# Performance work log

Hardware: AMD Instinct MI355X
Metric: run time of the kernel (lower is better)

Reference implementation:

```python
import jax, jax.numpy as jnp
import numpy as np

D_IN = 1024
D_OUT = 1024
NUM_HEADS = 16
HEAD_DIM = D_OUT // NUM_HEADS


def setup_inputs() -> dict:
    key = jax.random.key(0)
    k_x, k_qkv, k_pw, k_pb = jax.random.split(key, 4)
    x = jax.random.normal(k_x, (2, 2048, D_IN), dtype=jnp.float32)
    # torch nn.Linear(d_in, 3*d_out, bias=False): weight [3*d_out, d_in]
    w_qkv = jax.random.normal(k_qkv, (3 * D_OUT, D_IN), dtype=jnp.float32) * (1.0 / np.sqrt(D_IN))
    # proj: nn.Linear(d_out, d_out) with bias
    w_proj = jax.random.normal(k_pw, (D_OUT, D_OUT), dtype=jnp.float32) * (1.0 / np.sqrt(D_OUT))
    b_proj = jax.random.normal(k_pb, (D_OUT,), dtype=jnp.float32) * 0.01
    return {"x": x, "w_qkv": w_qkv, "w_proj": w_proj, "b_proj": b_proj}


def reference(x, w_qkv, w_proj, b_proj):
    B, S, _ = x.shape
    # fused QKV projection: [B,S,3*D_OUT]
    qkv = jnp.einsum('bsd,ed->bse', x, w_qkv)
    qkv = qkv.reshape(B, S, 3, NUM_HEADS, HEAD_DIM)
    q, k, v = jnp.moveaxis(qkv, 2, 0)  # each [B,S,H,Dh]
    scale = 1.0 / jnp.sqrt(jnp.asarray(HEAD_DIM, dtype=x.dtype))
    # scores [B,H,S,S]
    scores = jnp.einsum('bqhd,bkhd->bhqk', q, k) * scale
    causal = jnp.tril(jnp.ones((S, S), dtype=bool))
    scores = jnp.where(causal, scores, jnp.asarray(-jnp.inf, dtype=scores.dtype))
    attn = jax.nn.softmax(scores, axis=-1)
    ctx = jnp.einsum('bhqk,bkhd->bqhd', attn, v)  # [B,S,H,Dh]
    ctx = ctx.reshape(B, S, D_OUT)
    return jnp.einsum('bsd,ed->bse', ctx, w_proj) + b_proj
```

## Files before the change

kernel.cpp:

```cpp
#include <hip/hip_runtime.h>
#include <hip/hip_bf16.h>
#include <cstdint>

#define B_SZ   2
#define S_LEN  2048
#define NH     16
#define NT     32
#define LDA    72

using f32x4 = __attribute__((ext_vector_type(4))) float;
typedef __bf16 bf16x8 __attribute__((ext_vector_type(8)));
typedef __bf16 bf16x4 __attribute__((ext_vector_type(4)));

__device__ inline float bf2f(unsigned short u) {
    union { unsigned int i; float f; } v; v.i = ((unsigned int)u) << 16; return v.f;
}
__device__ inline unsigned short f2bf(float f) {
    union { float f; unsigned int i; } v; v.f = f;
    unsigned int r = v.i + 0x7fff + ((v.i >> 16) & 1);
    return (unsigned short)(r >> 16);
}
__device__ inline f32x4 mfma16(bf16x8 a, bf16x8 b, f32x4 c) {
    return __builtin_amdgcn_mfma_f32_16x16x32_bf16(a, b, c, 0, 0, 0);
}
__device__ inline void stC(float* C, size_t idx, float v)  { C[idx] = v; }
__device__ inline void stC(__bf16* C, size_t idx, float v) { ((unsigned short*)C)[idx] = f2bf(v); }

__global__ __launch_bounds__(256) void f2b2_kernel(
    const float* __restrict__ a, int na4, __bf16* __restrict__ outa,
    const float* __restrict__ b, int nb4, __bf16* __restrict__ outb)
{
    int i = blockIdx.x * blockDim.x + threadIdx.x;
    const float* src; __bf16* dst; int idx;
    if (i < na4)           { src = a; dst = outa; idx = i; }
    else if (i < na4 + nb4){ src = b; dst = outb; idx = i - na4; }
    else return;
    float4 v = ((const float4*)src)[idx];
    ushort4 o;
    o.x = f2bf(v.x); o.y = f2bf(v.y); o.z = f2bf(v.z); o.w = f2bf(v.w);
    ((ushort4*)dst)[idx] = o;
}

__global__ __launch_bounds__(256) void f2b_kernel(
    const float* __restrict__ in, __bf16* __restrict__ out, int n4)
{
    int i = blockIdx.x * blockDim.x + threadIdx.x;
    if (i < n4) {
        float4 v = ((const float4*)in)[i];
        ushort4 o;
        o.x = f2bf(v.x); o.y = f2bf(v.y); o.z = f2bf(v.z); o.w = f2bf(v.w);
        ((ushort4*)out)[i] = o;
    }
}

template <typename TO, int HAS_BIAS>
__global__ __launch_bounds__(256) void gemm128(
    const __bf16* __restrict__ A, const __bf16* __restrict__ W,
    const float* __restrict__ bias, TO* __restrict__ C,
    int M, int N, int K)
{
    __shared__ __bf16 Alds[2][128 * 32];
    __shared__ __bf16 Blds[2][128 * 32];
    const int tid  = threadIdx.x, lane = tid & 63, w = tid >> 6;
    const int c16  = lane & 15, quad = lane >> 4;
    const int mBase = blockIdx.y * 128, nBase = blockIdx.x * 128;
    const int moff = (w & 1) * 64, noff = (w >> 1) * 64;

    f32x4 acc[4][4];
#pragma unroll
    for (int i = 0; i < 4; ++i)
#pragma unroll
        for (int j = 0; j < 4; ++j) acc[i][j] = (f32x4){0.f, 0.f, 0.f, 0.f};

    auto stage = [&](int buf, int k0) {
#pragma unroll
        for (int p = 0; p < 2; ++p) {
            const int linear = p * 256 + tid;
            const int row = linear >> 2;
            const int seg = (linear & 3) ^ (row & 3);
            const int lbase = (p * 256 + w * 64) * 8;
            const __bf16* ga = A + (size_t)(mBase + row) * K + k0 + seg * 8;
            const __bf16* gb = W + (size_t)(nBase + row) * K + k0 + seg * 8;
            __builtin_amdgcn_global_load_lds(
                (const __attribute__((address_space(1))) void*)ga,
                (__attribute__((address_space(3))) void*)(&Alds[buf][lbase]), 16, 0, 0);
            __builtin_amdgcn_global_load_lds(
                (const __attribute__((address_space(1))) void*)gb,
                (__attribute__((address_space(3))) void*)(&Blds[buf][lbase]), 16, 0, 0);
        }
    };

    stage(0, 0);
    int cur = 0;
    for (int k0 = 0; k0 < K; k0 += 32) {
        __syncthreads();
        if (k0 + 32 < K) stage(cur ^ 1, k0 + 32);

        bf16x8 af[4], bw[4];
#pragma unroll
        for (int i = 0; i < 4; ++i) {
            const int rowA = moff + i * 16 + c16;
            af[i] = *(const bf16x8*)&Alds[cur][rowA * 32 + ((quad ^ (rowA & 3)) << 3)];
            const int rowB = noff + i * 16 + c16;
            bw[i] = *(const bf16x8*)&Blds[cur][rowB * 32 + ((quad ^ (rowB & 3)) << 3)];
        }
#pragma unroll
        for (int i = 0; i < 4; ++i)
#pragma unroll
            for (int j = 0; j < 4; ++j)
                acc[i][j] = mfma16(af[i], bw[j], acc[i][j]);
        cur ^= 1;
    }

#pragma unroll
    for (int j = 0; j < 4; ++j) {
        const int col = nBase + noff + j * 16 + c16;
        const float bv = HAS_BIAS ? bias[col] : 0.f;
#pragma unroll
        for (int i = 0; i < 4; ++i)
#pragma unroll
            for (int r = 0; r < 4; ++r) {
                const int row = mBase + moff + i * 16 + quad * 4 + r;
                stC(C, (size_t)row * N + col, acc[i][j][r] + bv);
            }
    }
}

template <typename TO, int HAS_BIAS>
__global__ __launch_bounds__(256) void gemm64(
    const __bf16* __restrict__ A, const __bf16* __restrict__ W,
    const float* __restrict__ bias, TO* __restrict__ C,
    int M, int N, int K)
{
    __shared__ __bf16 Alds[2][64 * 32];
    __shared__ __bf16 Blds[2][128 * 32];
    const int tid  = threadIdx.x, lane = tid & 63, w = tid >> 6;
    const int c16  = lane & 15, quad = lane >> 4;
    const int mBase = blockIdx.y * 64, nBase = blockIdx.x * 128;
    const int moff = (w & 1) * 32, noff = (w >> 1) * 64;

    f32x4 acc[2][4];
#pragma unroll
    for (int i = 0; i < 2; ++i)
#pragma unroll
        for (int j = 0; j < 4; ++j) acc[i][j] = (f32x4){0.f, 0.f, 0.f, 0.f};

    auto stage = [&](int buf, int k0) {
        {
            const int row = tid >> 2;
            const int seg = (tid & 3) ^ (row & 3);
            const int lbase = (w * 64) * 8;
            const __bf16* ga = A + (size_t)(mBase + row) * K + k0 + seg * 8;
            __builtin_amdgcn_global_load_lds(
                (const __attribute__((address_space(1))) void*)ga,
                (__attribute__((address_space(3))) void*)(&Alds[buf][lbase]), 16, 0, 0);
        }
#pragma unroll
        for (int p = 0; p < 2; ++p) {
            const int linear = p * 256 + tid;
            const int row = linear >> 2;
            const int seg = (linear & 3) ^ (row & 3);
            const int lbase = (p * 256 + w * 64) * 8;
            const __bf16* gb = W + (size_t)(nBase + row) * K + k0 + seg * 8;
            __builtin_amdgcn_global_load_lds(
                (const __attribute__((address_space(1))) void*)gb,
                (__attribute__((address_space(3))) void*)(&Blds[buf][lbase]), 16, 0, 0);
        }
    };

    stage(0, 0);
    int cur = 0;
    for (int k0 = 0; k0 < K; k0 += 32) {
        __syncthreads();
        if (k0 + 32 < K) stage(cur ^ 1, k0 + 32);

        bf16x8 af[2], bw[4];
#pragma unroll
        for (int i = 0; i < 2; ++i) {
            const int rowA = moff + i * 16 + c16;
            af[i] = *(const bf16x8*)&Alds[cur][rowA * 32 + ((quad ^ (rowA & 3)) << 3)];
        }
#pragma unroll
        for (int j = 0; j < 4; ++j) {
            const int rowB = noff + j * 16 + c16;
            bw[j] = *(const bf16x8*)&Blds[cur][rowB * 32 + ((quad ^ (rowB & 3)) << 3)];
        }
#pragma unroll
        for (int i = 0; i < 2; ++i)
#pragma unroll
            for (int j = 0; j < 4; ++j)
                acc[i][j] = mfma16(af[i], bw[j], acc[i][j]);
        cur ^= 1;
    }

#pragma unroll
    for (int j = 0; j < 4; ++j) {
        const int col = nBase + noff + j * 16 + c16;
        const float bv = HAS_BIAS ? bias[col] : 0.f;
#pragma unroll
        for (int i = 0; i < 2; ++i)
#pragma unroll
            for (int r = 0; r < 4; ++r) {
                const int row = mBase + moff + i * 16 + quad * 4 + r;
                stC(C, (size_t)row * N + col, acc[i][j][r] + bv);
            }
    }
}

__global__ __launch_bounds__(256) void attn(
    const __bf16* __restrict__ qkv, __bf16* __restrict__ ctx,
    float* __restrict__ opart, float* __restrict__ lpart)
{
    __shared__ __bf16 Qs[64 * LDA];
    __shared__ __bf16 Ks[64 * LDA];
    __shared__ __bf16 Vs[64 * LDA];
    __shared__ __bf16 Ps[64 * LDA];

    const int tid  = threadIdx.x;
    const int lane = tid & 63;
    const int w    = tid >> 6;
    const int c16  = lane & 15;
    const int quad = lane >> 4;
    const int bh = blockIdx.x, b = bh >> 4, h = bh & 15;
    const int y  = blockIdx.y;

    int qt, c0, c1, seg;
    bool split;
    if (y < 16)      { qt = 16 + y; const int half = (qt + 2) >> 1; c0 = 0;    c1 = half;   split = true;  seg = 0; }
    else if (y < 32) { qt = y;      const int half = (qt + 2) >> 1; c0 = half; c1 = qt + 1; split = true;  seg = 1; }
    else             { qt = 47 - y; c0 = 0; c1 = qt + 1; split = false; seg = 0; }
    const int qBase = qt * 64;
    const int segIdx = split ? ((bh * 16 + (qt - 16)) * 2 + seg) : 0;

    const float QS = 0.125f * 1.4426950408889634f;

    const int krow0 = tid >> 3;
    const int kd0   = (tid & 7) * 8;
    const int c16t = tid & 15;
    const int jh   = (tid >> 4) & 1;
    const int dblk = tid >> 5;

    const size_t rowB = (size_t)b * S_LEN;
    const __bf16* kp0 = qkv + (rowB + c0 * 64 + krow0) * 3072 + 1024 + h * 64 + kd0;
    const __bf16* kp1 = kp0 + (size_t)32 * 3072;
    const __bf16* vp0 = qkv + (rowB + c0 * 64 + 2 * jh * 16 + c16t) * 3072 + 2048 + h * 64 + dblk * 8;
    const __bf16* vp1 = vp0 + (size_t)16 * 3072;

    uint4 kr0 = *(const uint4*)kp0;
    uint4 kr1 = *(const uint4*)kp1;
    uint4 vr0 = *(const uint4*)vp0;
    uint4 vr1 = *(const uint4*)vp1;

#pragma unroll
    for (int p = 0; p < 2; ++p) {
        const int linear = p * 256 + tid;
        const int row = linear >> 3;
        const int d0 = (linear & 7) * 8;
        const __bf16* g = qkv + (rowB + qBase + row) * 3072 + h * 64 + d0;
        uint4 raw = *(const uint4*)g;
        const unsigned short* u = (const unsigned short*)&raw;
        unsigned short tmp[8];
#pragma unroll
        for (int jj = 0; jj < 8; ++jj) tmp[jj] = f2bf(bf2f(u[jj]) * QS);
        *(uint4*)&Qs[row * LDA + d0] = *(const uint4*)tmp;
    }
    __syncthreads();

    const bf16x8 aq0 = *(const bf16x8*)&Qs[(w * 16 + c16) * LDA + quad * 8];
    const bf16x8 aq1 = *(const bf16x8*)&Qs[(w * 16 + c16) * LDA + 32 + quad * 8];

    float l_r[4] = {0.f, 0.f, 0.f, 0.f};
    f32x4 acc_o[4];
#pragma unroll
    for (int j = 0; j < 4; ++j) acc_o[j] = (f32x4){0.f, 0.f, 0.f, 0.f};

    for (int cc = c0; cc < c1; ++cc) {
        *(uint4*)&Ks[krow0 * LDA + kd0]        = kr0;
        *(uint4*)&Ks[(krow0 + 32) * LDA + kd0] = kr1;
        {
            const unsigned short* e1 = (const unsigned short*)&vr0;
            const unsigned short* e2 = (const unsigned short*)&vr1;
#pragma unroll
            for (int d = 0; d < 8; ++d) {
                const unsigned pack = (unsigned)e1[d] | ((unsigned)e2[d] << 16);
                *(unsigned*)&Vs[(dblk * 8 + d) * LDA + c16t * 4 + 2 * jh] = pack;
            }
        }
        __syncthreads();

        if (cc + 1 < c1) {
            kp0 += (size_t)64 * 3072; kp1 += (size_t)64 * 3072;
            vp0 += (size_t)64 * 3072; vp1 += (size_t)64 * 3072;
            kr0 = *(const uint4*)kp0;
            kr1 = *(const uint4*)kp1;
            vr0 = *(const uint4*)vp0;
            vr1 = *(const uint4*)vp1;
        }

        f32x4 sc[4];
#pragma unroll
        for (int j = 0; j < 4; ++j) sc[j] = (f32x4){0.f, 0.f, 0.f, 0.f};
#pragma unroll
        for (int j = 0; j < 4; ++j) {
            bf16x8 bk0 = *(const bf16x8*)&Ks[(j * 16 + c16) * LDA + quad * 8];
            bf16x8 bk1 = *(const bf16x8*)&Ks[(j * 16 + c16) * LDA + 32 + quad * 8];
            sc[j] = mfma16(aq0, bk0, sc[j]);
            sc[j] = mfma16(aq1, bk1, sc[j]);
        }

        if (cc == qt) {
#pragma unroll
            for (int j = 0; j < 4; ++j) {
                const int key = cc * 64 + j * 16 + c16;
#pragma unroll
                for (int r = 0; r < 4; ++r) {
                    const int q = qBase + w * 16 + quad * 4 + r;
                    if (key > q) sc[j][r] = -1e30f;
                }
            }
        }

        float p_[4][4];
#pragma unroll
        for (int j = 0; j < 4; ++j)
#pragma unroll
            for (int r = 0; r < 4; ++r)
                p_[j][r] = exp2f(sc[j][r]);
#pragma unroll
        for (int r = 0; r < 4; ++r)
            l_r[r] += (p_[0][r] + p_[1][r]) + (p_[2][r] + p_[3][r]);

#pragma unroll
        for (int r = 0; r < 4; ++r) {
            bf16x4 pb;
            pb[0] = (__bf16)p_[0][r]; pb[1] = (__bf16)p_[1][r];
            pb[2] = (__bf16)p_[2][r]; pb[3] = (__bf16)p_[3][r];
            *(bf16x4*)&Ps[(w * 16 + quad * 4 + r) * LDA + c16 * 4] = pb;
        }

        bf16x8 ap0 = *(const bf16x8*)&Ps[(w * 16 + c16) * LDA + quad * 8];
        bf16x8 ap1 = *(const bf16x8*)&Ps[(w * 16 + c16) * LDA + 32 + quad * 8];
#pragma unroll
        for (int j = 0; j < 4; ++j) {
            bf16x8 bv0 = *(const bf16x8*)&Vs[(j * 16 + c16) * LDA + quad * 8];
            bf16x8 bv1 = *(const bf16x8*)&Vs[(j * 16 + c16) * LDA + 32 + quad * 8];
            acc_o[j] = mfma16(ap0, bv0, acc_o[j]);
            acc_o[j] = mfma16(ap1, bv1, acc_o[j]);
        }
        __syncthreads();
    }

    if (!split) {
#pragma unroll
        for (int r = 0; r < 4; ++r) {
            float l = l_r[r];
            l += __shfl_xor(l, 1);
            l += __shfl_xor(l, 2);
            l += __shfl_xor(l, 4);
            l += __shfl_xor(l, 8);
            const float inv = 1.0f / l;
            const size_t rowO = (rowB + qBase + w * 16 + quad * 4 + r) * 1024 + h * 64;
#pragma unroll
            for (int j = 0; j < 4; ++j)
                ctx[rowO + j * 16 + c16] = (__bf16)(acc_o[j][r] * inv);
        }
    } else {
        float* ob = opart + (size_t)segIdx * 4096;
#pragma unroll
        for (int r = 0; r < 4; ++r) {
            float l = l_r[r];
            l += __shfl_xor(l, 1);
            l += __shfl_xor(l, 2);
            l += __shfl_xor(l, 4);
            l += __shfl_xor(l, 8);
            const int qrow = w * 16 + quad * 4 + r;
            if (c16 == 0) lpart[segIdx * 64 + qrow] = l;
#pragma unroll
            for (int j = 0; j < 4; ++j)
                ob[qrow * 64 + j * 16 + c16] = acc_o[j][r];
        }
    }
}

__global__ __launch_bounds__(256) void attn_combine(
    const float* __restrict__ opart, const float* __restrict__ lpart,
    __bf16* __restrict__ ctx)
{
    const int blk = blockIdx.x;
    const int bh = blk >> 4, t = blk & 15;
    const int b = bh >> 4, h = bh & 15;
    const int qt = 16 + t;
    const int tid = threadIdx.x;
    const int q  = tid >> 2;
    const int d0 = (tid & 3) * 16;
    const int segA = blk * 2, segB = segA + 1;
    const float* oa = opart + (size_t)segA * 4096 + q * 64 + d0;
    const float* obp = opart + (size_t)segB * 4096 + q * 64 + d0;
    const float inv = 1.0f / (lpart[segA * 64 + q] + lpart[segB * 64 + q]);
    unsigned short outv[16];
#pragma unroll
    for (int i = 0; i < 4; ++i) {
        float4 a = ((const float4*)oa)[i];
        float4 c = ((const float4*)obp)[i];
        outv[4 * i + 0] = f2bf((a.x + c.x) * inv);
        outv[4 * i + 1] = f2bf((a.y + c.y) * inv);
        outv[4 * i + 2] = f2bf((a.z + c.z) * inv);
        outv[4 * i + 3] = f2bf((a.w + c.w) * inv);
    }
    __bf16* dst = ctx + ((size_t)(b * S_LEN + qt * 64 + q)) * 1024 + h * 64 + d0;
    *(uint4*)dst       = *(const uint4*)&outv[0];
    *(uint4*)(dst + 8) = *(const uint4*)&outv[8];
}

extern "C" void kernel_launch(void* const* d_in, const int* in_sizes, int n_in,
                              void* d_out, int out_size, void* d_ws, size_t ws_size,
                              hipStream_t stream) {
    const float* x      = (const float*)d_in[0];
    const float* w_qkv  = (const float*)d_in[1];
    const float* w_proj = (const float*)d_in[2];
    const float* b_proj = (const float*)d_in[3];
    float* out = (float*)d_out;

    __bf16* qkvb = (__bf16*)d_ws;
    __bf16* xb   = qkvb + (size_t)4096 * 3072;
    __bf16* wqb  = xb + (size_t)4096 * 1024;
    __bf16* ctxb = xb;
    __bf16* wpb  = wqb;
    float*  lpart = (float*)(wqb + (size_t)1024 * 1024);
    float* opart = out;

    const int M = B_SZ * S_LEN;
    const int nx4 = 4096 * 1024 / 4, nq4 = 3072 * 1024 / 4, np4 = 1024 * 1024 / 4;

    f2b2_kernel<<<(nx4 + nq4 + 255) / 256, 256, 0, stream>>>(x, nx4, xb, w_qkv, nq4, wqb);

    gemm128<__bf16, 0><<<dim3(3072 / 128, M / 128), 256, 0, stream>>>(
        xb, wqb, nullptr, qkvb, M, 3072, 1024);

    f2b_kernel<<<(np4 + 255) / 256, 256, 0, stream>>>(w_proj, wpb, np4);

    attn<<<dim3(B_SZ * NH, 48), 256, 0, stream>>>(qkvb, ctxb, opart, lpart);
    attn_combine<<<B_SZ * NH * 16, 256, 0, stream>>>(opart, lpart, ctxb);

    gemm64<float, 1><<<dim3(1024 / 128, M / 64), 256, 0, stream>>>(
        ctxb, wpb, b_proj, out, M, 1024, 1024);
}
```

Before: 185.4 us.

## Compute transposed scores and pass P to PV MFMA via lane shuffles

Swaps the MFMA operand order so each lane holds scores for a single query row, masks with the transposed index mapping, and packs the probabilities into bf16 pairs. The shared-memory round trip for P is replaced with cross-lane shuffles that assemble the A operand for the PV MFMA directly in registers. The row-sum reduction becomes a single scalar per lane reduced across quads. This removes the Ps LDS buffer and its store/load traffic, at the cost of 16 shuffles plus selects per tile.

```diff
diff --git a/kernel.cpp b/kernel.cpp
--- a/kernel.cpp
+++ b/kernel.cpp
@@ -22,6 +22,12 @@
 }
 __device__ inline f32x4 mfma16(bf16x8 a, bf16x8 b, f32x4 c) {
     return __builtin_amdgcn_mfma_f32_16x16x32_bf16(a, b, c, 0, 0, 0);
+}
+__device__ inline unsigned pack_bf16x2(float lo, float hi) {
+    float2 f2; f2.x = lo; f2.y = hi;
+    __hip_bfloat162 bb = __float22bfloat162_rn(f2);
+    union { __hip_bfloat162 b; unsigned u; } cv; cv.b = bb;
+    return cv.u;
 }
 __device__ inline void stC(float* C, size_t idx, float v)  { C[idx] = v; }
 __device__ inline void stC(__bf16* C, size_t idx, float v) { ((unsigned short*)C)[idx] = f2bf(v); }
@@ -214,7 +220,6 @@
     __shared__ __bf16 Qs[64 * LDA];
     __shared__ __bf16 Ks[64 * LDA];
     __shared__ __bf16 Vs[64 * LDA];
-    __shared__ __bf16 Ps[64 * LDA];
 
     const int tid  = threadIdx.x;
     const int lane = tid & 63;
@@ -269,7 +274,7 @@
     const bf16x8 aq0 = *(const bf16x8*)&Qs[(w * 16 + c16) * LDA + quad * 8];
     const bf16x8 aq1 = *(const bf16x8*)&Qs[(w * 16 + c16) * LDA + 32 + quad * 8];
 
-    float l_r[4] = {0.f, 0.f, 0.f, 0.f};
+    float lp = 0.f;
     f32x4 acc_o[4];
 #pragma unroll
     for (int j = 0; j < 4; ++j) acc_o[j] = (f32x4){0.f, 0.f, 0.f, 0.f};
@@ -304,17 +309,17 @@
         for (int j = 0; j < 4; ++j) {
             bf16x8 bk0 = *(const bf16x8*)&Ks[(j * 16 + c16) * LDA + quad * 8];
             bf16x8 bk1 = *(const bf16x8*)&Ks[(j * 16 + c16) * LDA + 32 + quad * 8];
-            sc[j] = mfma16(aq0, bk0, sc[j]);
-            sc[j] = mfma16(aq1, bk1, sc[j]);
+            sc[j] = mfma16(bk0, aq0, sc[j]);
+            sc[j] = mfma16(bk1, aq1, sc[j]);
         }
 
         if (cc == qt) {
+            const int q = qBase + w * 16 + c16;
 #pragma unroll
             for (int j = 0; j < 4; ++j) {
-                const int key = cc * 64 + j * 16 + c16;
 #pragma unroll
                 for (int r = 0; r < 4; ++r) {
-                    const int q = qBase + w * 16 + quad * 4 + r;
+                    const int key = cc * 64 + j * 16 + quad * 4 + r;
                     if (key > q) sc[j][r] = -1e30f;
                 }
             }
@@ -327,19 +332,36 @@
             for (int r = 0; r < 4; ++r)
                 p_[j][r] = exp2f(sc[j][r]);
 #pragma unroll
-        for (int r = 0; r < 4; ++r)
-            l_r[r] += (p_[0][r] + p_[1][r]) + (p_[2][r] + p_[3][r]);
-
+        for (int j = 0; j < 4; ++j)
+            lp += (p_[j][0] + p_[j][1]) + (p_[j][2] + p_[j][3]);
+
+        unsigned Wp[2][4];
 #pragma unroll
         for (int r = 0; r < 4; ++r) {
-            bf16x4 pb;
-            pb[0] = (__bf16)p_[0][r]; pb[1] = (__bf16)p_[1][r];
-            pb[2] = (__bf16)p_[2][r]; pb[3] = (__bf16)p_[3][r];
-            *(bf16x4*)&Ps[(w * 16 + quad * 4 + r) * LDA + c16 * 4] = pb;
-        }
-
-        bf16x8 ap0 = *(const bf16x8*)&Ps[(w * 16 + c16) * LDA + quad * 8];
-        bf16x8 ap1 = *(const bf16x8*)&Ps[(w * 16 + c16) * LDA + 32 + quad * 8];
+            Wp[0][r] = pack_bf16x2(p_[0][r], p_[1][r]);
+            Wp[1][r] = pack_bf16x2(p_[2][r], p_[3][r]);
+        }
+
+        const int q0 = quad & 1, q1 = quad >> 1;
+        const int src0 = 16 * q1 + c16;
+        const int src1 = 32 + 16 * q1 + c16;
+        unsigned a0w[4], a1w[4];
+#pragma unroll
+        for (int t = 0; t < 4; ++t) {
+            const int j2 = t & 1, rb = t >> 1;
+            unsigned lo0 = (unsigned)__shfl((int)Wp[j2][rb],     src0);
+            unsigned hi0 = (unsigned)__shfl((int)Wp[j2][2 + rb], src0);
+            a0w[t] = q0 ? hi0 : lo0;
+            unsigned lo1 = (unsigned)__shfl((int)Wp[j2][rb],     src1);
+            unsigned hi1 = (unsigned)__shfl((int)Wp[j2][2 + rb], src1);
+            a1w[t] = q0 ? hi1 : lo1;
+        }
+        union { unsigned u[4]; bf16x8 v; } U0, U1;
+#pragma unroll
+        for (int t = 0; t < 4; ++t) { U0.u[t] = a0w[t]; U1.u[t] = a1w[t]; }
+        const bf16x8 ap0 = U0.v;
+        const bf16x8 ap1 = U1.v;
+
 #pragma unroll
         for (int j = 0; j < 4; ++j) {
             bf16x8 bv0 = *(const bf16x8*)&Vs[(j * 16 + c16) * LDA + quad * 8];
@@ -350,15 +372,13 @@
         __syncthreads();
     }
 
+    lp += __shfl_xor(lp, 16);
+    lp += __shfl_xor(lp, 32);
+
     if (!split) {
 #pragma unroll
         for (int r = 0; r < 4; ++r) {
-            float l = l_r[r];
-            l += __shfl_xor(l, 1);
-            l += __shfl_xor(l, 2);
-            l += __shfl_xor(l, 4);
-            l += __shfl_xor(l, 8);
-            const float inv = 1.0f / l;
+            const float inv = 1.0f / __shfl(lp, quad * 4 + r);
             const size_t rowO = (rowB + qBase + w * 16 + quad * 4 + r) * 1024 + h * 64;
 #pragma unroll
             for (int j = 0; j < 4; ++j)
@@ -366,15 +386,10 @@
         }
     } else {
         float* ob = opart + (size_t)segIdx * 4096;
+        if (quad == 0) lpart[segIdx * 64 + w * 16 + c16] = lp;
 #pragma unroll
         for (int r = 0; r < 4; ++r) {
-            float l = l_r[r];
-            l += __shfl_xor(l, 1);
-            l += __shfl_xor(l, 2);
-            l += __shfl_xor(l, 4);
-            l += __shfl_xor(l, 8);
             const int qrow = w * 16 + quad * 4 + r;
-            if (c16 == 0) lpart[segIdx * 64 + qrow] = l;
 #pragma unroll
             for (int j = 0; j < 4; ++j)
                 ob[qrow * 64 + j * 16 + c16] = acc_o[j][r];
```

Measured after the change: 191.1 us. +3.0%, slower.
